# Kernel tuning notes

Measured on AMD Instinct MI355X. Metric: run time of the kernel, lower is better.

Reference implementation:

```python
import jax, jax.numpy as jnp
import numpy as np

LEN_C = 1024
LR = 0.01
GAMMA = 0.999
R, S, E = 4, 4, 4


def setup_inputs() -> dict:
    key = jax.random.key(0)
    k1, k2, k3 = jax.random.split(key, 3)
    Fx = jax.random.normal(k1, (R, S, E, LEN_C), dtype=jnp.float32)
    Dis = jax.random.normal(k2, (E, LEN_C), dtype=jnp.float32)
    initial_weights = jax.random.normal(k3, (R, S, LEN_C), dtype=jnp.float32) * 0.02
    return {"Fx": Fx, "Dis": Dis, "initial_weights": initial_weights}


def reference(Fx, Dis, initial_weights):
    len_c = Fx.shape[-1]
    # --- first_grad: one-step adaptation gradient (detached in original torch code) ---
    w0 = jax.lax.stop_gradient(initial_weights)
    anti = jnp.einsum('rsen,rsn->e', Fx, w0)           # [E]
    error = Dis[:, -1] - anti                           # [E]
    # d/dw of sum_e error_e^2 with error = Dis - Fx.w  =>  -2 * Fx^T error
    weights_grad = jax.lax.stop_gradient(-2.0 * jnp.einsum('rsen,e->rsn', Fx, error))
    control_weights = initial_weights - 0.5 * LR * weights_grad  # [R,S,N]
    # --- build_delay_line, vectorized Toeplitz gather:
    # Fx_extend[t, r, s, e, n] = Fx[r, s, e, t-n] if t >= n else 0
    t = jnp.arange(len_c)
    idx = t[:, None] - t[None, :]                       # [T, N]
    mask = idx >= 0
    safe_idx = jnp.where(mask, idx, 0)
    Fx_ext = jnp.where(mask, Fx[..., safe_idx], jnp.float32(0.0))  # [R,S,E,T,N]
    # --- adaptive_filtering: sum over r, s, n ---
    anti_noise_matrix = jnp.einsum('rsetn,rsn->te', Fx_ext, control_weights)  # [T,E]
    gamma_vector = jnp.power(jnp.float32(GAMMA), (len_c - 1 - t).astype(jnp.float32))
    return anti_noise_matrix, gamma_vector
```

## Files before the change

kernel.cpp:

```cpp
#include <hip/hip_runtime.h>

#define LEN_C 1024
#define LR_F 0.01f
#define GAMMA_F 0.999f

__global__ __launch_bounds__(256) void k_err(const float* __restrict__ Fx,
                                             const float* __restrict__ w0,
                                             float* __restrict__ anti_ws,
                                             float* __restrict__ out) {
    const int rs = blockIdx.x;
    const int tid = threadIdx.x;

    __shared__ float sPart[4][4];

    if (rs < 4) {
        int g = (rs << 8) + tid;
        out[4 * LEN_C + g] = powf(GAMMA_F, (float)(LEN_C - 1 - g));
    }

    const float4* w4 = (const float4*)(w0 + rs * LEN_C);
    const float4* f4 = (const float4*)(Fx + rs * 4 * LEN_C);
    float4 wv = w4[tid];
    float4 f0 = f4[tid];
    float4 f1 = f4[256 + tid];
    float4 f2 = f4[512 + tid];
    float4 f3 = f4[768 + tid];

    float a0 = f0.x * wv.x + f0.y * wv.y + f0.z * wv.z + f0.w * wv.w;
    float a1 = f1.x * wv.x + f1.y * wv.y + f1.z * wv.z + f1.w * wv.w;
    float a2 = f2.x * wv.x + f2.y * wv.y + f2.z * wv.z + f2.w * wv.w;
    float a3 = f3.x * wv.x + f3.y * wv.y + f3.z * wv.z + f3.w * wv.w;

    #pragma unroll
    for (int off = 32; off > 0; off >>= 1) {
        a0 += __shfl_down(a0, off, 64);
        a1 += __shfl_down(a1, off, 64);
        a2 += __shfl_down(a2, off, 64);
        a3 += __shfl_down(a3, off, 64);
    }
    const int w = tid >> 6, l = tid & 63;
    if (l == 0) { sPart[w][0] = a0; sPart[w][1] = a1; sPart[w][2] = a2; sPart[w][3] = a3; }
    __syncthreads();
    if (tid < 4) {
        float p = sPart[0][tid] + sPart[1][tid] + sPart[2][tid] + sPart[3][tid];
        atomicAdd(&anti_ws[tid], p);
    }
}

__global__ __launch_bounds__(256) void k_conv(const float* __restrict__ Fx,
                                              const float* __restrict__ Dis,
                                              const float* __restrict__ w0,
                                              const float* __restrict__ anti_ws,
                                              float* __restrict__ out) {
    const int bid = blockIdx.x;
    const int tid = threadIdx.x;
    const int g = bid & 3;
    const int r = (bid >> 2) % 40;
    const int e = bid / 160;

    int Tb, Nb;
    if (r < 4)       { Tb = 0; Nb = r; }
    else if (r < 12) { Tb = 1; Nb = r - 4; }
    else if (r < 24) { Tb = 2; Nb = r - 12; }
    else             { Tb = 3; Nb = r - 24; }
    const int T0 = Tb * 256, N0 = Nb * 64;
    const int B = T0 - N0 - 63;

    __shared__ __align__(16) float sFx[4 * 320];
    __shared__ __align__(16) float sCw[4 * 64];
    __shared__ float sErr[4];

    #pragma unroll
    for (int rr = 0; rr < 4; ++rr) {
        const float* src = Fx + ((g * 4 + rr) * 4 + e) * LEN_C;
        for (int m = tid; m < 320; m += 256) {
            int k = B + m;
            sFx[rr * 320 + m] = ((unsigned)k < (unsigned)LEN_C) ? src[k] : 0.f;
        }
    }

    const int rr = tid >> 6, j = tid & 63;
    const int rs2 = g * 4 + rr, n = N0 + j;
    const float* cbase = Fx + rs2 * 4 * LEN_C + n;
    float cf0 = cbase[0];
    float cf1 = cbase[LEN_C];
    float cf2 = cbase[2 * LEN_C];
    float cf3 = cbase[3 * LEN_C];
    float cwv = w0[rs2 * LEN_C + n];

    if (tid < 4) sErr[tid] = Dis[tid * LEN_C + (LEN_C - 1)] - anti_ws[tid];
    __syncthreads();

    sCw[rr * 64 + j] = cwv + LR_F * (cf0 * sErr[0] + cf1 * sErr[1] +
                                     cf2 * sErr[2] + cf3 * sErr[3]);
    __syncthreads();

    const int w = tid >> 6, l = tid & 63;
    const int i0 = l * 4;
    float acc0 = 0.f, acc1 = 0.f, acc2 = 0.f, acc3 = 0.f;
    {
        const float* crow = sCw + w * 64;
        const float* frow = sFx + w * 320;
        int M = i0 + 60;
        float4 flo = *(const float4*)(frow + M);
        float4 fhi = *(const float4*)(frow + M + 4);
        #pragma unroll
        for (int jb = 0; jb < 16; ++jb) {
            float4 c = *(const float4*)(crow + (jb << 2));
            float v0 = flo.x, v1 = flo.y, v2 = flo.z, v3 = flo.w;
            float v4 = fhi.x, v5 = fhi.y, v6 = fhi.z;
            acc0 += v3 * c.x + v2 * c.y + v1 * c.z + v0 * c.w;
            acc1 += v4 * c.x + v3 * c.y + v2 * c.z + v1 * c.w;
            acc2 += v5 * c.x + v4 * c.y + v3 * c.z + v2 * c.w;
            acc3 += v6 * c.x + v5 * c.y + v4 * c.z + v3 * c.w;
            fhi = flo;
            M -= 4;
            if (jb < 15) flo = *(const float4*)(frow + M);
        }
    }

    __syncthreads();
    float* sred = sFx;
    sred[w * 256 + i0 + 0] = acc0;
    sred[w * 256 + i0 + 1] = acc1;
    sred[w * 256 + i0 + 2] = acc2;
    sred[w * 256 + i0 + 3] = acc3;
    __syncthreads();
    float sum = sred[tid] + sred[256 + tid] + sred[512 + tid] + sred[768 + tid];
    atomicAdd(&out[(T0 + tid) * 4 + e], sum);
}

extern "C" void kernel_launch(void* const* d_in, const int* in_sizes, int n_in,
                              void* d_out, int out_size, void* d_ws, size_t ws_size,
                              hipStream_t stream) {
    const float* Fx  = (const float*)d_in[0];
    const float* Dis = (const float*)d_in[1];
    const float* w0  = (const float*)d_in[2];
    float* out = (float*)d_out;
    float* anti_ws = (float*)d_ws;

    k_err<<<16, 256, 0, stream>>>(Fx, w0, anti_ws, out);
    k_conv<<<640, 256, 0, stream>>>(Fx, Dis, w0, anti_ws, out);
}
```

Before: 68.59 us.

## Fuse error-reduction kernel into convolution kernel with grid-level flag synchronization

```diff
diff --git a/kernel.cpp b/kernel.cpp
--- a/kernel.cpp
+++ b/kernel.cpp
@@ -3,55 +3,13 @@
 #define LEN_C 1024
 #define LR_F 0.01f
 #define GAMMA_F 0.999f
+#define DONE_MAGIC 0x5ABC6DEFu
 
-__global__ __launch_bounds__(256) void k_err(const float* __restrict__ Fx,
-                                             const float* __restrict__ w0,
-                                             float* __restrict__ anti_ws,
-                                             float* __restrict__ out) {
-    const int rs = blockIdx.x;
-    const int tid = threadIdx.x;
-
-    __shared__ float sPart[4][4];
-
-    if (rs < 4) {
-        int g = (rs << 8) + tid;
-        out[4 * LEN_C + g] = powf(GAMMA_F, (float)(LEN_C - 1 - g));
-    }
-
-    const float4* w4 = (const float4*)(w0 + rs * LEN_C);
-    const float4* f4 = (const float4*)(Fx + rs * 4 * LEN_C);
-    float4 wv = w4[tid];
-    float4 f0 = f4[tid];
-    float4 f1 = f4[256 + tid];
-    float4 f2 = f4[512 + tid];
-    float4 f3 = f4[768 + tid];
-
-    float a0 = f0.x * wv.x + f0.y * wv.y + f0.z * wv.z + f0.w * wv.w;
-    float a1 = f1.x * wv.x + f1.y * wv.y + f1.z * wv.z + f1.w * wv.w;
-    float a2 = f2.x * wv.x + f2.y * wv.y + f2.z * wv.z + f2.w * wv.w;
-    float a3 = f3.x * wv.x + f3.y * wv.y + f3.z * wv.z + f3.w * wv.w;
-
-    #pragma unroll
-    for (int off = 32; off > 0; off >>= 1) {
-        a0 += __shfl_down(a0, off, 64);
-        a1 += __shfl_down(a1, off, 64);
-        a2 += __shfl_down(a2, off, 64);
-        a3 += __shfl_down(a3, off, 64);
-    }
-    const int w = tid >> 6, l = tid & 63;
-    if (l == 0) { sPart[w][0] = a0; sPart[w][1] = a1; sPart[w][2] = a2; sPart[w][3] = a3; }
-    __syncthreads();
-    if (tid < 4) {
-        float p = sPart[0][tid] + sPart[1][tid] + sPart[2][tid] + sPart[3][tid];
-        atomicAdd(&anti_ws[tid], p);
-    }
-}
-
-__global__ __launch_bounds__(256) void k_conv(const float* __restrict__ Fx,
-                                              const float* __restrict__ Dis,
-                                              const float* __restrict__ w0,
-                                              const float* __restrict__ anti_ws,
-                                              float* __restrict__ out) {
+__global__ __launch_bounds__(256) void k_fused(const float* __restrict__ Fx,
+                                               const float* __restrict__ Dis,
+                                               const float* __restrict__ w0,
+                                               float* __restrict__ ws,
+                                               float* __restrict__ out) {
     const int bid = blockIdx.x;
     const int tid = threadIdx.x;
     const int g = bid & 3;
@@ -66,9 +24,36 @@
     const int T0 = Tb * 256, N0 = Nb * 64;
     const int B = T0 - N0 - 63;
 
+    float* part = ws;
+    unsigned* done = (unsigned*)(ws + 64);
+
     __shared__ __align__(16) float sFx[4 * 320];
     __shared__ __align__(16) float sCw[4 * 64];
     __shared__ float sErr[4];
+
+    if (bid < 16) {
+        const int rs = bid, lane = tid & 63, ew = tid >> 6;
+        const float4* f4 = (const float4*)(Fx + (rs * 4 + ew) * LEN_C);
+        const float4* w4 = (const float4*)(w0 + rs * LEN_C);
+        float a = 0.f;
+        #pragma unroll
+        for (int k = 0; k < 4; ++k) {
+            float4 f = f4[lane + 64 * k];
+            float4 wv = w4[lane + 64 * k];
+            a += f.x * wv.x + f.y * wv.y + f.z * wv.z + f.w * wv.w;
+        }
+        #pragma unroll
+        for (int off = 32; off > 0; off >>= 1) a += __shfl_down(a, off, 64);
+        if (lane == 0) {
+            __hip_atomic_store(&part[rs * 4 + ew], a, __ATOMIC_RELAXED,
+                               __HIP_MEMORY_SCOPE_AGENT);
+            __threadfence();
+        }
+        __syncthreads();
+        if (tid == 0)
+            __hip_atomic_store(&done[rs], DONE_MAGIC, __ATOMIC_RELEASE,
+                               __HIP_MEMORY_SCOPE_AGENT);
+    }
 
     #pragma unroll
     for (int rr = 0; rr < 4; ++rr) {
@@ -88,7 +73,26 @@
     float cf3 = cbase[3 * LEN_C];
     float cwv = w0[rs2 * LEN_C + n];
 
-    if (tid < 4) sErr[tid] = Dis[tid * LEN_C + (LEN_C - 1)] - anti_ws[tid];
+    if ((unsigned)(bid - 16) < 4u) {
+        int gi = ((bid - 16) << 8) + tid;
+        out[4 * LEN_C + gi] = powf(GAMMA_F, (float)(LEN_C - 1 - gi));
+    }
+
+    if (tid < 16) {
+        while (__hip_atomic_load(&done[tid], __ATOMIC_ACQUIRE,
+                                 __HIP_MEMORY_SCOPE_AGENT) != DONE_MAGIC)
+            __builtin_amdgcn_s_sleep(2);
+    }
+    __syncthreads();
+
+    if (tid < 4) {
+        float anti = 0.f;
+        #pragma unroll
+        for (int rs = 0; rs < 16; ++rs)
+            anti += __hip_atomic_load(&part[rs * 4 + tid], __ATOMIC_RELAXED,
+                                      __HIP_MEMORY_SCOPE_AGENT);
+        sErr[tid] = Dis[tid * LEN_C + (LEN_C - 1)] - anti;
+    }
     __syncthreads();
 
     sCw[rr * 64 + j] = cwv + LR_F * (cf0 * sErr[0] + cf1 * sErr[1] +
@@ -137,8 +141,7 @@
     const float* Dis = (const float*)d_in[1];
     const float* w0  = (const float*)d_in[2];
     float* out = (float*)d_out;
-    float* anti_ws = (float*)d_ws;
+    float* ws  = (float*)d_ws;
 
-    k_err<<<16, 256, 0, stream>>>(Fx, w0, anti_ws, out);
-    k_conv<<<640, 256, 0, stream>>>(Fx, Dis, w0, anti_ws, out);
+    k_fused<<<640, 256, 0, stream>>>(Fx, Dis, w0, ws, out);
 }
```

Result: slower. 81.11 us (+18.3%).
